# Performance work log

Measured on AMD Instinct MI355X. Metric: run time of the kernel, lower is better.

The kernel has to match this reference:

```python
import jax, jax.numpy as jnp
import numpy as np

R_HEADS = 4   # read heads
CELL = 64     # cell_size (word width)
MEM = 512     # nr_cells
DELTA = 1e-6


def _content_weights(mem, keys, strengths):
    # mem: (B,M,Wc), keys: (B,K,Wc), strengths: (B,K) -> (B,K,M)
    mn = jnp.linalg.norm(mem, axis=2, keepdims=True) + DELTA
    kn = jnp.linalg.norm(keys, axis=2, keepdims=True) + DELTA
    d = jnp.einsum('bkw,bmw->bkm', keys / kn, mem / mn)  # cosine similarity
    return jax.nn.softmax(d * strengths[:, :, None], axis=2)


def _allocate(usage):
    # usage: (B,M) -> allocation weighting (B,M)
    B = usage.shape[0]
    u = DELTA + (1.0 - DELTA) * usage
    idx = jnp.argsort(u, axis=1)                               # ascending usage
    sorted_u = jnp.take_along_axis(u, idx, axis=1)
    prod_su = jnp.cumprod(
        jnp.concatenate([jnp.ones((B, 1), u.dtype), sorted_u], axis=1), axis=1)[:, :-1]
    sorted_alloc = (1.0 - sorted_u) * prod_su
    inv = jnp.argsort(idx, axis=1)                             # inverse permutation
    return jnp.take_along_axis(sorted_alloc, inv, axis=1)


def dnc_forward(x, W_ih, b_ih, W_hh, b_hh, W_out, b_out, W_int, b_int, W_mem, b_mem):
    B, T, IN = x.shape
    H = W_hh.shape[1]
    r, w, m = R_HEADS, CELL, MEM
    eye_mask = 1.0 - jnp.eye(m, dtype=x.dtype)  # zero link-matrix diagonal

    def step(carry, x_t):
        h, c, mem, link, prec, read_w, write_w, usage, last_read = carry
        # controller LSTM cell (torch gate order i,f,g,o)
        inp = jnp.concatenate([x_t, last_read], axis=1)
        gates = inp @ W_ih.T + b_ih + h @ W_hh.T + b_hh
        gi, gf, gg, go = jnp.split(gates, 4, axis=1)
        c = jax.nn.sigmoid(gf) * c + jax.nn.sigmoid(gi) * jnp.tanh(gg)
        h = jax.nn.sigmoid(go) * jnp.tanh(c)
        out = h @ W_out.T + b_out
        xi = h @ W_int.T + b_int  # interface vector, size r*w+3w+5r+3
        # parse interface
        o = r * w
        read_keys = jnp.tanh(xi[:, :r * w].reshape(B, r, w))
        read_str = jax.nn.softplus(xi[:, o:o + r]); o += r
        write_key = jnp.tanh(xi[:, o:o + w].reshape(B, 1, w)); o += w
        write_str = jax.nn.softplus(xi[:, o:o + 1]); o += 1
        erase = jax.nn.sigmoid(xi[:, o:o + w].reshape(B, 1, w)); o += w
        write_vec = jnp.tanh(xi[:, o:o + w].reshape(B, 1, w)); o += w
        free_gates = jax.nn.sigmoid(xi[:, o:o + r]); o += r
        alloc_gate = jax.nn.sigmoid(xi[:, o:o + 1]); o += 1
        write_gate = jax.nn.sigmoid(xi[:, o:o + 1]); o += 1
        read_modes = jax.nn.softmax(xi[:, o:o + 3 * r].reshape(B, r, 3), axis=-1)

        # ---- write ----
        usage = usage + (1 - usage) * (1 - jnp.prod(1 - write_w, axis=1))
        psi = jnp.prod(1 - free_gates[:, :, None] * read_w, axis=1)
        usage = usage * psi
        wcw = _content_weights(mem, write_key, write_str)      # (B,1,M)
        alloc = _allocate(usage)[:, None, :]                   # (B,1,M)
        ag = alloc_gate[:, :, None]
        write_w = write_gate[:, :, None] * (ag * alloc + (1 - ag) * wcw)
        reset = jnp.prod(1 - write_w[:, :, :, None] * erase[:, :, None, :], axis=1)  # (B,M,Wc)
        mem = mem * reset + jnp.einsum('bkm,bkw->bmw', write_w, write_vec)
        ww = write_w[:, 0]                                     # (B,M), single write head
        L = link[:, 0]
        L = (1 - ww[:, :, None] - ww[:, None, :]) * L + ww[:, :, None] * prec[:, 0][:, None, :]
        L = L * eye_mask
        link = L[:, None]
        prec = (1 - jnp.sum(write_w, axis=2, keepdims=True)) * prec + write_w

        # ---- read ----
        cw = _content_weights(mem, read_keys, read_str)        # (B,R,M)
        fwd = jnp.einsum('bij,brj->bri', L, read_w)
        bwd = jnp.einsum('bri,bij->brj', read_w, L)
        read_w = (read_modes[:, :, 0:1] * bwd
                  + read_modes[:, :, 1:2] * fwd
                  + read_modes[:, :, 2:3] * cw)
        read_vecs = jnp.einsum('brm,bmw->brw', read_w, mem).reshape(B, r * w)
        y = jnp.concatenate([out, read_vecs], axis=1) @ W_mem.T + b_mem
        return (h, c, mem, link, prec, read_w, write_w, usage, read_vecs), y

    z = lambda *s: jnp.zeros(s, x.dtype)
    carry0 = (z(B, H), z(B, H), z(B, m, w), z(B, 1, m, m), z(B, 1, m),
              z(B, r, m), z(B, 1, m), z(B, m), z(B, r * w))
    _, ys = jax.lax.scan(step, carry0, jnp.swapaxes(x, 0, 1))
    return jnp.swapaxes(ys, 0, 1)  # (B,T,IN)


def setup_inputs() -> dict:
    key = jax.random.key(0)
    ks = jax.random.split(key, 12)
    B, T, IN, H = 16, 32, 256, 512
    r, w = R_HEADS, CELL
    iface = w * r + 3 * w + 5 * r + 3  # 471
    s = 0.05
    return {
        'x': jax.random.normal(ks[0], (B, T, IN), jnp.float32),
        'W_ih': jax.random.normal(ks[1], (4 * H, IN + r * w), jnp.float32) * s,
        'b_ih': jax.random.normal(ks[2], (4 * H,), jnp.float32) * s,
        'W_hh': jax.random.normal(ks[3], (4 * H, H), jnp.float32) * s,
        'b_hh': jax.random.normal(ks[4], (4 * H,), jnp.float32) * s,
        'W_out': jax.random.normal(ks[5], (H, H), jnp.float32) * s,
        'b_out': jax.random.normal(ks[6], (H,), jnp.float32) * s,
        'W_int': jax.random.normal(ks[7], (iface, H), jnp.float32) * s,
        'b_int': jax.random.normal(ks[8], (iface,), jnp.float32) * s,
        'W_mem': jax.random.normal(ks[9], (IN, r * w + H), jnp.float32) * s,
        'b_mem': jax.random.normal(ks[10], (IN,), jnp.float32) * s,
    }


def reference(x, W_ih, b_ih, W_hh, b_hh, W_out, b_out, W_int, b_int, W_mem, b_mem):
    return dnc_forward(x, W_ih, b_ih, W_hh, b_hh, W_out, b_out, W_int, b_int, W_mem, b_mem)
```

## Files before the change

### kernel.cpp

```cpp
#include <hip/hip_runtime.h>
#include <math.h>

#define NB 16
#define NT 256
#define NWG 256
#define TT 32
#define INP 256
#define HH 512
#define RH 4
#define CWID 64
#define MM 512
#define IFACE 471
#define DELTA 1e-6f
#define AP 516

__device__ __align__(16) float g_h[2][NB][HH];
__device__ __align__(16) float g_c[NB][HH];
__device__ __align__(16) float g_lr[NB][INP];
__device__ __align__(16) float g_usage[NB][MM];
__device__ __align__(16) float g_ww[NB][MM];
__device__ __align__(16) float g_prec[2][NB][MM];
__device__ __align__(16) float g_rw[NB][RH][MM];
__device__ __align__(16) float g_mem[NB][MM][CWID];
__device__ __align__(16) float g_L[NB][MM][MM];
__device__ __align__(16) float g_out[NB][HH];
__device__ __align__(16) float g_xi[NB][HH];
__device__ __align__(16) float g_rkn[NB][RH][CWID];
__device__ __align__(16) float g_rs[NB][RH];
__device__ __align__(16) float g_erase[NB][CWID];
__device__ __align__(16) float g_wv[NB][CWID];
__device__ __align__(16) float g_modes[NB][RH][3];
__device__ __align__(16) float g_fwd[NB][RH][MM];
__device__ __align__(16) float g_bwdp[NB][16][RH][MM];
__device__ __align__(16) float g_e[NB][RH][MM];
__device__ __align__(16) float g_cwsp[NB][16][RH];
__device__ __align__(16) float g_rvp[NB][16][RH][CWID];

struct P {
  const float *x, *W_ih, *b_ih, *W_hh, *b_hh, *W_out, *b_out, *W_int, *b_int, *W_mem, *b_mem;
  float* y;
};

__device__ __forceinline__ float sigf(float x)  { return 1.f / (1.f + __expf(-x)); }
__device__ __forceinline__ float splus(float x) { return fmaxf(x, 0.f) + log1pf(__expf(-fabsf(x))); }

__device__ __forceinline__ void zfill(float* a, long n) {
  const long stride = (long)gridDim.x * blockDim.x;
  for (long i = (long)blockIdx.x * blockDim.x + threadIdx.x; i < n; i += stride) a[i] = 0.f;
}

__global__ void __launch_bounds__(NT) k_init() {
  zfill(&g_h[0][0][0], 2L*NB*HH);
  zfill(&g_c[0][0], (long)NB*HH);
  zfill(&g_lr[0][0], (long)NB*INP);
  zfill(&g_usage[0][0], (long)NB*MM);
  zfill(&g_ww[0][0], (long)NB*MM);
  zfill(&g_prec[0][0][0], 2L*NB*MM);
  zfill(&g_rw[0][0][0], (long)NB*RH*MM);
  zfill(&g_mem[0][0][0], (long)NB*MM*CWID);
  zfill(&g_L[0][0][0], (long)NB*MM*MM);
}

__global__ void __launch_bounds__(NT) k_ph1(P p, int t) {
  __shared__ __align__(16) float sm[14432];
  float* As  = sm;
  float* Ws  = sm + 16*AP;
  float* red = sm + 24*AP;
  const int tid = threadIdx.x;
  const int j0  = 2 * (int)blockIdx.x;
  const int op  = tid & 3;
  const int bq  = (tid >> 2) & 3;
  const int ks  = tid >> 4;
  const float (*hsrc)[HH] = g_h[t & 1];
  float acc0[4] = {0.f,0.f,0.f,0.f};
  float acc1[4] = {0.f,0.f,0.f,0.f};
  for (int pass = 0; pass < 2; ++pass) {
    if (pass == 0) {
      for (int idx = tid; idx < NB*INP; idx += NT) {
        int b = idx >> 8, k = idx & 255;
        As[b*AP + k] = p.x[((size_t)b*TT + t)*INP + k];
      }
      for (int idx = tid; idx < NB*INP; idx += NT) {
        int b = idx >> 8, k = idx & 255;
        As[b*AP + INP + k] = g_lr[b][k];
      }
    } else {
      for (int idx = tid; idx < NB*HH; idx += NT) {
        int b = idx >> 9, k = idx & 511;
        As[b*AP + k] = hsrc[b][k];
      }
    }
    const float* Wsrc = pass ? p.W_hh : p.W_ih;
    for (int idx = tid; idx < 8*512; idx += NT) {
      int ro = idx >> 9, k = idx & 511;
      int row = (ro >> 1)*HH + j0 + (ro & 1);
      Ws[ro*AP + k] = Wsrc[(size_t)row*512 + k];
    }
    __syncthreads();
    const int k0 = ks * 32;
    #pragma unroll
    for (int k4 = 0; k4 < 32; k4 += 4) {
      const float4 w0 = *(const float4*)&Ws[(op*2+0)*AP + k0 + k4];
      const float4 w1 = *(const float4*)&Ws[(op*2+1)*AP + k0 + k4];
      #pragma unroll
      for (int bb = 0; bb < 4; ++bb) {
        const float4 a = *(const float4*)&As[(bq*4+bb)*AP + k0 + k4];
        acc0[bb] += a.x*w0.x + a.y*w0.y + a.z*w0.z + a.w*w0.w;
        acc1[bb] += a.x*w1.x + a.y*w1.y + a.z*w1.z + a.w*w1.w;
      }
    }
    __syncthreads();
  }
  #pragma unroll
  for (int bb = 0; bb < 4; ++bb) {
    red[(op*2+0)*256 + (bq*4+bb)*16 + ks] = acc0[bb];
    red[(op*2+1)*256 + (bq*4+bb)*16 + ks] = acc1[bb];
  }
  __syncthreads();
  if (tid < 128) {
    int o = tid >> 4, b = tid & 15;
    float s = 0.f;
    #pragma unroll
    for (int q = 0; q < 16; ++q) s += red[o*256 + b*16 + q];
    int row = (o >> 1)*HH + j0 + (o & 1);
    red[o*256 + b*16] = s + p.b_ih[row] + p.b_hh[row];
  }
  __syncthreads();
  if (tid < 32) {
    int jj = tid >> 4, b = tid & 15;
    int j  = j0 + jj;
    float gi = red[(0+jj)*256 + b*16];
    float gf = red[(2+jj)*256 + b*16];
    float gg = red[(4+jj)*256 + b*16];
    float go = red[(6+jj)*256 + b*16];
    float c0 = g_c[b][j];
    float cn = sigf(gf)*c0 + sigf(gi)*tanhf(gg);
    float hn = sigf(go)*tanhf(cn);
    g_c[b][j] = cn;
    g_h[(t+1) & 1][b][j] = hn;
  }
}

__global__ void __launch_bounds__(NT) k_ph2(P p, int t) {
  __shared__ __align__(16) float sm[10576];
  float* hs  = sm;
  float* Ws  = sm + 16*AP;
  float* red = sm + 20*AP;
  const int tid = threadIdx.x;
  const int o0  = 4 * (int)blockIdx.x;
  const float (*hcur)[HH] = g_h[(t+1) & 1];
  for (int idx = tid; idx < NB*HH; idx += NT) {
    int b = idx >> 9, k = idx & 511;
    hs[b*AP + k] = hcur[b][k];
  }
  for (int idx = tid; idx < 4*512; idx += NT) {
    int oi = idx >> 9, k = idx & 511;
    int o = o0 + oi;
    float v = 0.f;
    if (o < HH)              v = p.W_out[(size_t)o*512 + k];
    else if (o < HH + IFACE) v = p.W_int[(size_t)(o - HH)*512 + k];
    Ws[oi*AP + k] = v;
  }
  __syncthreads();
  {
    const int b = tid & 15, oi = (tid >> 4) & 3, ks = tid >> 6;
    const int k0 = ks * 128;
    float acc = 0.f;
    #pragma unroll 8
    for (int k4 = 0; k4 < 128; k4 += 4) {
      const float4 a  = *(const float4*)&hs[b*AP + k0 + k4];
      const float4 wv = *(const float4*)&Ws[oi*AP + k0 + k4];
      acc += a.x*wv.x + a.y*wv.y + a.z*wv.z + a.w*wv.w;
    }
    red[(oi*16 + b)*4 + ks] = acc;
  }
  __syncthreads();
  if (tid < 64) {
    int oi = tid >> 4, b = tid & 15;
    int base = (oi*16 + b)*4;
    float s = red[base] + red[base+1] + red[base+2] + red[base+3];
    int o = o0 + oi;
    if (o < HH) g_out[b][o] = s + p.b_out[o];
    else if (o < HH + IFACE) g_xi[b][o - HH] = s + p.b_int[o - HH];
  }
}

__global__ void __launch_bounds__(512) k_ph3(int pp) {
  __shared__ __align__(16) float sm[4152];
  const int b = (int)blockIdx.x, tid = threadIdx.x;
  float* xi_l = sm;
  float* wkn  = sm + 472;
  float* sc   = sm + 536;
  float* u_l  = sm + 552;
  float* wcw  = sm + 1064;
  float* su   = sm + 1576;
  float* cA   = sm + 2088;
  float* cB   = sm + 2600;
  float* wwl  = sm + 3112;
  float* red  = sm + 3624;
  int*   rnk  = (int*)(sm + 3640);

  for (int i = tid; i < IFACE; i += 512) xi_l[i] = g_xi[b][i];
  __syncthreads();
  {
    const int wv = tid >> 6, v = tid & 63;
    if (wv < 4) {
      float kv = tanhf(xi_l[wv*64 + v]);
      float ss = kv * kv;
      #pragma unroll
      for (int d = 1; d < 64; d <<= 1) ss += __shfl_xor(ss, d, 64);
      g_rkn[b][wv][v] = kv / (sqrtf(ss) + DELTA);
      if (v == 0) { float s_ = splus(xi_l[256 + wv]); sc[wv] = s_; g_rs[b][wv] = s_; }
    } else if (wv == 4) {
      float kv = tanhf(xi_l[260 + v]);
      float ss = kv * kv;
      #pragma unroll
      for (int d = 1; d < 64; d <<= 1) ss += __shfl_xor(ss, d, 64);
      wkn[v] = kv / (sqrtf(ss) + DELTA);
    } else if (wv == 5) {
      g_erase[b][v] = sigf(xi_l[325 + v]);
    } else if (wv == 6) {
      g_wv[b][v] = tanhf(xi_l[389 + v]);
    } else {
      if (v < 4)       sc[4 + v] = sigf(xi_l[453 + v]);
      else if (v == 4) sc[8] = sigf(xi_l[457]);
      else if (v == 5) sc[9] = sigf(xi_l[458]);
      else if (v == 6) sc[10] = splus(xi_l[324]);
      else if (v >= 8 && v < 12) {
        int r = v - 8;
        float a0 = xi_l[459 + r*3], a1 = xi_l[459 + r*3 + 1], a2 = xi_l[459 + r*3 + 2];
        float mx = fmaxf(a0, fmaxf(a1, a2));
        float e0 = __expf(a0 - mx), e1 = __expf(a1 - mx), e2 = __expf(a2 - mx);
        float si = e0 + e1 + e2;
        g_modes[b][r][0] = e0/si; g_modes[b][r][1] = e1/si; g_modes[b][r][2] = e2/si;
      }
    }
  }
  __syncthreads();
  {
    float uo = g_usage[b][tid];
    float wwp = g_ww[b][tid];
    float psi = 1.f;
    #pragma unroll
    for (int r = 0; r < RH; ++r) psi *= 1.f - sc[4+r]*g_rw[b][r][tid];
    float un = (uo + (1.f - uo)*wwp) * psi;
    g_usage[b][tid] = un;
    u_l[tid] = DELTA + (1.f - DELTA)*un;
  }
  {
    float dot = 0.f, nn = 0.f;
    const float* mr = &g_mem[b][tid][0];
    #pragma unroll
    for (int v4 = 0; v4 < CWID; v4 += 4) {
      float4 m4 = *(const float4*)&mr[v4];
      dot += m4.x*wkn[v4] + m4.y*wkn[v4+1] + m4.z*wkn[v4+2] + m4.w*wkn[v4+3];
      nn  += m4.x*m4.x + m4.y*m4.y + m4.z*m4.z + m4.w*m4.w;
    }
    wcw[tid] = (dot / (sqrtf(nn) + DELTA)) * sc[10];
  }
  __syncthreads();
  {
    const int wv = tid >> 6, v = tid & 63;
    float x0 = wcw[tid];
    float mx = x0;
    #pragma unroll
    for (int d = 1; d < 64; d <<= 1) mx = fmaxf(mx, __shfl_xor(mx, d, 64));
    if (v == 0) red[wv] = mx;
    __syncthreads();
    float gmx = red[0];
    #pragma unroll
    for (int q = 1; q < 8; ++q) gmx = fmaxf(gmx, red[q]);
    float e0 = __expf(x0 - gmx);
    float ss = e0;
    #pragma unroll
    for (int d = 1; d < 64; d <<= 1) ss += __shfl_xor(ss, d, 64);
    if (v == 0) red[8 + wv] = ss;
    __syncthreads();
    float tot = red[8];
    #pragma unroll
    for (int q = 9; q < 16; ++q) tot += red[q];
    wcw[tid] = e0 / tot;
  }
  __syncthreads();
  {
    const float u0 = u_l[tid];
    int cnt = 0;
    for (int j = 0; j < MM; j += 8) {
      const float4 a = *(const float4*)&u_l[j];
      const float4 c = *(const float4*)&u_l[j + 4];
      cnt += (a.x < u0) || (a.x == u0 && (j+0) < tid);
      cnt += (a.y < u0) || (a.y == u0 && (j+1) < tid);
      cnt += (a.z < u0) || (a.z == u0 && (j+2) < tid);
      cnt += (a.w < u0) || (a.w == u0 && (j+3) < tid);
      cnt += (c.x < u0) || (c.x == u0 && (j+4) < tid);
      cnt += (c.y < u0) || (c.y == u0 && (j+5) < tid);
      cnt += (c.z < u0) || (c.z == u0 && (j+6) < tid);
      cnt += (c.w < u0) || (c.w == u0 && (j+7) < tid);
    }
    rnk[tid] = cnt;
    su[cnt] = u0;
  }
  __syncthreads();
  cA[tid] = tid ? su[tid - 1] : 1.f;
  __syncthreads();
  {
    float* src = cA;
    float* dst = cB;
    for (int d = 1; d < MM; d <<= 1) {
      float v = src[tid];
      if (tid >= d) v *= src[tid - d];
      dst[tid] = v;
      __syncthreads();
      float* tmp = src; src = dst; dst = tmp;
    }
    float ag = sc[8], wgt = sc[9];
    float alloc = (1.f - u_l[tid]) * src[rnk[tid]];
    float wn = wgt * (ag*alloc + (1.f - ag)*wcw[tid]);
    wwl[tid] = wn;
    g_ww[b][tid] = wn;
  }
  __syncthreads();
  {
    const int wv = tid >> 6, v = tid & 63;
    float s2 = wwl[tid];
    #pragma unroll
    for (int d = 1; d < 64; d <<= 1) s2 += __shfl_xor(s2, d, 64);
    if (v == 0) red[wv] = s2;
    __syncthreads();
    float sww = red[0];
    #pragma unroll
    for (int q = 1; q < 8; ++q) sww += red[q];
    g_prec[1 - pp][b][tid] = (1.f - sww)*g_prec[pp][b][tid] + wwl[tid];
  }
}

__global__ void __launch_bounds__(NT) k_ph4(int pp) {
  __shared__ __align__(16) float sm[6608];
  const int w = (int)blockIdx.x, tid = threadIdx.x;
  const int b = w >> 4, s = w & 15, i0 = s * 32;
  float* pl   = sm;
  float* wwl  = sm + 512;
  float* rwl  = sm + 1024;
  float* el   = sm + 3072;
  float* wvl  = sm + 3136;
  float* rknl = sm + 3200;
  float* rs4  = sm + 3456;
  float* fp   = sm + 3472;
  float* mt   = sm + 4496;
  float* nrm  = sm + 6576;

  for (int i = tid; i < MM; i += NT) { pl[i] = g_prec[pp][b][i]; wwl[i] = g_ww[b][i]; }
  for (int i = tid; i < RH*MM; i += NT) rwl[i] = g_rw[b][i >> 9][i & 511];
  for (int i = tid; i < CWID; i += NT) { el[i] = g_erase[b][i]; wvl[i] = g_wv[b][i]; }
  for (int i = tid; i < RH*CWID; i += NT) rknl[i] = g_rkn[b][i >> 6][i & 63];
  if (tid < 4) rs4[tid] = g_rs[b][tid];
  __syncthreads();
  {
    const int ii = tid >> 3, js = tid & 7;
    const int i = i0 + ii;
    const float wwi = wwl[i];
    float f0=0.f, f1=0.f, f2=0.f, f3=0.f;
    float* Lrow = &g_L[b][i][0];
    #pragma unroll
    for (int step = 0; step < 16; ++step) {
      const int col = js*64 + ((js*8 + step*4) & 63);
      float4 l4 = *(float4*)&Lrow[col];
      float lv[4] = {l4.x, l4.y, l4.z, l4.w};
      #pragma unroll
      for (int q = 0; q < 4; ++q) {
        const int jq = col + q;
        float lnv = (1.f - wwi - wwl[jq]) * lv[q] + wwi * pl[jq];
        if (jq == i) lnv = 0.f;
        lv[q] = lnv;
        f0 += lnv * rwl[jq];
        f1 += lnv * rwl[512 + jq];
        f2 += lnv * rwl[1024 + jq];
        f3 += lnv * rwl[1536 + jq];
      }
      *(float4*)&Lrow[col] = make_float4(lv[0], lv[1], lv[2], lv[3]);
    }
    fp[(ii*8 + js)*4 + 0] = f0;
    fp[(ii*8 + js)*4 + 1] = f1;
    fp[(ii*8 + js)*4 + 2] = f2;
    fp[(ii*8 + js)*4 + 3] = f3;
  }
  __syncthreads();
  if (tid < 128) {
    int ii = tid >> 2, r = tid & 3;
    float sY = 0.f;
    #pragma unroll
    for (int js = 0; js < 8; ++js) sY += fp[(ii*8 + js)*4 + r];
    g_fwd[b][r][i0 + ii] = sY;
  }
  {
    const int j = tid * 2;
    float a00=0,a01=0,a10=0,a11=0,a20=0,a21=0,a30=0,a31=0;
    #pragma unroll 4
    for (int ii2 = 0; ii2 < 32; ++ii2) {
      const int i = i0 + ii2;
      const float2 l2 = *(const float2*)&g_L[b][i][j];
      const float r0 = rwl[i], r1 = rwl[512+i], r2 = rwl[1024+i], r3 = rwl[1536+i];
      a00 += r0*l2.x; a01 += r0*l2.y;
      a10 += r1*l2.x; a11 += r1*l2.y;
      a20 += r2*l2.x; a21 += r2*l2.y;
      a30 += r3*l2.x; a31 += r3*l2.y;
    }
    g_bwdp[b][s][0][j] = a00; g_bwdp[b][s][0][j+1] = a01;
    g_bwdp[b][s][1][j] = a10; g_bwdp[b][s][1][j+1] = a11;
    g_bwdp[b][s][2][j] = a20; g_bwdp[b][s][2][j+1] = a21;
    g_bwdp[b][s][3][j] = a30; g_bwdp[b][s][3][j+1] = a31;
  }
  for (int idx = tid; idx < 32*CWID; idx += NT) {
    int ii = idx >> 6, v = idx & 63;
    int i = i0 + ii;
    float wwi = wwl[i];
    float mv = g_mem[b][i][v];
    float mn = mv * (1.f - wwi*el[v]) + wwi*wvl[v];
    g_mem[b][i][v] = mn;
    mt[ii*65 + v] = mn;
  }
  __syncthreads();
  {
    int ii = tid >> 3, js = tid & 7;
    float nn = 0.f;
    #pragma unroll
    for (int q = 0; q < 8; ++q) { float mv = mt[ii*65 + js*8 + q]; nn += mv*mv; }
    fp[(ii*8 + js)*4] = nn;
  }
  __syncthreads();
  if (tid < 32) {
    float nn = 0.f;
    #pragma unroll
    for (int q = 0; q < 8; ++q) nn += fp[(tid*8 + q)*4];
    nrm[tid] = sqrtf(nn) + DELTA;
  }
  __syncthreads();
  {
    int ii = tid >> 3, js = tid & 7;
    float p0=0,p1=0,p2=0,p3=0;
    #pragma unroll
    for (int q = 0; q < 8; ++q) {
      float mv = mt[ii*65 + js*8 + q];
      p0 += mv * rknl[ 0 + js*8 + q];
      p1 += mv * rknl[ 64 + js*8 + q];
      p2 += mv * rknl[128 + js*8 + q];
      p3 += mv * rknl[192 + js*8 + q];
    }
    fp[(ii*8 + js)*4 + 0] = p0;
    fp[(ii*8 + js)*4 + 1] = p1;
    fp[(ii*8 + js)*4 + 2] = p2;
    fp[(ii*8 + js)*4 + 3] = p3;
  }
  __syncthreads();
  if (tid < 128) {
    int ii = tid >> 2, r = tid & 3;
    float d = 0.f;
    #pragma unroll
    for (int js = 0; js < 8; ++js) d += fp[(ii*8 + js)*4 + r];
    float e = __expf((d / nrm[ii]) * rs4[r]);
    g_e[b][r][i0 + ii] = e;
    mt[ii*4 + r] = e;
  }
  __syncthreads();
  if (tid < 4) {
    float ssum = 0.f;
    #pragma unroll
    for (int q = 0; q < 32; ++q) ssum += mt[q*4 + tid];
    g_cwsp[b][s][tid] = ssum;
  }
}

__global__ void __launch_bounds__(NT) k_ph5() {
  __shared__ __align__(16) float sm[144];
  const int w = (int)blockIdx.x, tid = threadIdx.x;
  const int b = w >> 4, s = w & 15, j0 = s * 32;
  float* Sr  = sm;
  float* rwt = sm + 16;
  if (tid < 4) {
    float ss = 0.f;
    #pragma unroll
    for (int q = 0; q < 16; ++q) ss += g_cwsp[b][q][tid];
    Sr[tid] = ss;
  }
  __syncthreads();
  if (tid < 128) {
    int jj = tid >> 2, r = tid & 3;
    int j = j0 + jj;
    float bw = 0.f;
    #pragma unroll
    for (int q = 0; q < 16; ++q) bw += g_bwdp[b][q][r][j];
    float fw = g_fwd[b][r][j];
    float cwv = g_e[b][r][j] / Sr[r];
    float rn = g_modes[b][r][0]*bw + g_modes[b][r][1]*fw + g_modes[b][r][2]*cwv;
    g_rw[b][r][j] = rn;
    rwt[r*32 + jj] = rn;
  }
  __syncthreads();
  {
    int r = tid >> 6, v = tid & 63;
    float acc = 0.f;
    #pragma unroll
    for (int jj = 0; jj < 32; ++jj) acc += rwt[r*32 + jj] * g_mem[b][j0 + jj][v];
    g_rvp[b][s][r][v] = acc;
  }
}

__global__ void __launch_bounds__(NT) k_ph6(P p, int t) {
  __shared__ __align__(16) float sm[1024];
  const int w = (int)blockIdx.x, tid = threadIdx.x;
  const int b = w >> 4, s = w & 15, o0 = s * 16;
  float* rv   = sm;
  float* outl = sm + 256;
  float* red  = sm + 768;
  {
    int r = tid >> 6, v = tid & 63;
    float acc = 0.f;
    #pragma unroll
    for (int q = 0; q < 16; ++q) acc += g_rvp[b][q][r][v];
    rv[r*64 + v] = acc;
    if (s == 0) g_lr[b][r*64 + v] = acc;
  }
  for (int k = tid; k < HH; k += NT) outl[k] = g_out[b][k];
  __syncthreads();
  {
    int oi = tid & 15, ks = tid >> 4;
    int o = o0 + oi;
    const float* wm = &p.W_mem[(size_t)o * 768];
    float acc = 0.f;
    for (int k = ks*48; k < ks*48 + 48; ++k) {
      float a = (k < HH) ? outl[k] : rv[k - HH];
      acc += a * wm[k];
    }
    red[oi*16 + ks] = acc;
  }
  __syncthreads();
  if (tid < 16) {
    int o = o0 + tid;
    float ss = 0.f;
    #pragma unroll
    for (int q = 0; q < 16; ++q) ss += red[tid*16 + q];
    p.y[((size_t)b*TT + t)*INP + o] = ss + p.b_mem[o];
  }
}

extern "C" void kernel_launch(void* const* d_in, const int* in_sizes, int n_in,
                              void* d_out, int out_size, void* d_ws, size_t ws_size,
                              hipStream_t stream) {
  (void)in_sizes; (void)n_in; (void)out_size; (void)d_ws; (void)ws_size;
  P p;
  p.x     = (const float*)d_in[0];
  p.W_ih  = (const float*)d_in[1];
  p.b_ih  = (const float*)d_in[2];
  p.W_hh  = (const float*)d_in[3];
  p.b_hh  = (const float*)d_in[4];
  p.W_out = (const float*)d_in[5];
  p.b_out = (const float*)d_in[6];
  p.W_int = (const float*)d_in[7];
  p.b_int = (const float*)d_in[8];
  p.W_mem = (const float*)d_in[9];
  p.b_mem = (const float*)d_in[10];
  p.y     = (float*)d_out;

  k_init<<<dim3(1024), dim3(NT), 0, stream>>>();
  for (int t = 0; t < TT; ++t) {
    const int pp = t & 1;
    k_ph1<<<dim3(NWG), dim3(NT), 0, stream>>>(p, t);
    k_ph2<<<dim3(NWG), dim3(NT), 0, stream>>>(p, t);
    k_ph3<<<dim3(NB),  dim3(512), 0, stream>>>(pp);
    k_ph4<<<dim3(NWG), dim3(NT), 0, stream>>>(pp);
    k_ph5<<<dim3(NWG), dim3(NT), 0, stream>>>();
    k_ph6<<<dim3(NWG), dim3(NT), 0, stream>>>(p, t);
  }
}
```

Baseline: 2.182 ms.

## Fuse read-weight and output phases, warp-scan cumprod, nontemporal weight loads

```diff
diff --git a/kernel.cpp b/kernel.cpp
--- a/kernel.cpp
+++ b/kernel.cpp
@@ -13,6 +13,8 @@
 #define IFACE 471
 #define DELTA 1e-6f
 #define AP 516
+
+#define NTLOAD(p_) __builtin_nontemporal_load(p_)
 
 __device__ __align__(16) float g_h[2][NB][HH];
 __device__ __align__(16) float g_c[NB][HH];
@@ -34,7 +36,6 @@
 __device__ __align__(16) float g_bwdp[NB][16][RH][MM];
 __device__ __align__(16) float g_e[NB][RH][MM];
 __device__ __align__(16) float g_cwsp[NB][16][RH];
-__device__ __align__(16) float g_rvp[NB][16][RH][CWID];
 
 struct P {
   const float *x, *W_ih, *b_ih, *W_hh, *b_hh, *W_out, *b_out, *W_int, *b_int, *W_mem, *b_mem;
@@ -94,7 +95,7 @@
     for (int idx = tid; idx < 8*512; idx += NT) {
       int ro = idx >> 9, k = idx & 511;
       int row = (ro >> 1)*HH + j0 + (ro & 1);
-      Ws[ro*AP + k] = Wsrc[(size_t)row*512 + k];
+      Ws[ro*AP + k] = NTLOAD(&Wsrc[(size_t)row*512 + k]);
     }
     __syncthreads();
     const int k0 = ks * 32;
@@ -157,8 +158,8 @@
     int oi = idx >> 9, k = idx & 511;
     int o = o0 + oi;
     float v = 0.f;
-    if (o < HH)              v = p.W_out[(size_t)o*512 + k];
-    else if (o < HH + IFACE) v = p.W_int[(size_t)(o - HH)*512 + k];
+    if (o < HH)              v = NTLOAD(&p.W_out[(size_t)o*512 + k]);
+    else if (o < HH + IFACE) v = NTLOAD(&p.W_int[(size_t)(o - HH)*512 + k]);
     Ws[oi*AP + k] = v;
   }
   __syncthreads();
@@ -194,7 +195,6 @@
   float* u_l  = sm + 552;
   float* wcw  = sm + 1064;
   float* su   = sm + 1576;
-  float* cA   = sm + 2088;
   float* cB   = sm + 2600;
   float* wwl  = sm + 3112;
   float* red  = sm + 3624;
@@ -301,20 +301,24 @@
     su[cnt] = u0;
   }
   __syncthreads();
-  cA[tid] = tid ? su[tid - 1] : 1.f;
-  __syncthreads();
-  {
-    float* src = cA;
-    float* dst = cB;
-    for (int d = 1; d < MM; d <<= 1) {
-      float v = src[tid];
-      if (tid >= d) v *= src[tid - d];
-      dst[tid] = v;
-      __syncthreads();
-      float* tmp = src; src = dst; dst = tmp;
-    }
+  {
+    const int lane = tid & 63, wv = tid >> 6;
+    float v = su[tid];
+    #pragma unroll
+    for (int d = 1; d < 64; d <<= 1) {
+      float m = __shfl_up(v, d, 64);
+      if (lane >= d) v *= m;
+    }
+    if (lane == 63) red[wv] = v;
+    __syncthreads();
+    float pre = 1.f;
+    for (int q = 0; q < wv; ++q) pre *= red[q];
+    cB[tid] = v * pre;
+    __syncthreads();
     float ag = sc[8], wgt = sc[9];
-    float alloc = (1.f - u_l[tid]) * src[rnk[tid]];
+    int rk = rnk[tid];
+    float excl = rk ? cB[rk - 1] : 1.f;
+    float alloc = (1.f - u_l[tid]) * excl;
     float wn = wgt * (ag*alloc + (1.f - ag)*wcw[tid]);
     wwl[tid] = wn;
     g_ww[b][tid] = wn;
@@ -470,57 +474,44 @@
   }
 }
 
-__global__ void __launch_bounds__(NT) k_ph5() {
-  __shared__ __align__(16) float sm[144];
+__global__ void __launch_bounds__(NT) k_ph56(P p, int t) {
+  __shared__ __align__(16) float sm[3072];
   const int w = (int)blockIdx.x, tid = threadIdx.x;
-  const int b = w >> 4, s = w & 15, j0 = s * 32;
-  float* Sr  = sm;
-  float* rwt = sm + 16;
-  if (tid < 4) {
+  const int b = w >> 4, s = w & 15, o0 = s * 16;
+  float* rwl  = sm;
+  float* rvl  = sm + 2048;
+  float* outl = sm + 2304;
+  float* red  = sm + 2816;
+  float Sr[4];
+  #pragma unroll
+  for (int r = 0; r < 4; ++r) {
     float ss = 0.f;
     #pragma unroll
-    for (int q = 0; q < 16; ++q) ss += g_cwsp[b][q][tid];
-    Sr[tid] = ss;
-  }
-  __syncthreads();
-  if (tid < 128) {
-    int jj = tid >> 2, r = tid & 3;
-    int j = j0 + jj;
-    float bw = 0.f;
-    #pragma unroll
-    for (int q = 0; q < 16; ++q) bw += g_bwdp[b][q][r][j];
-    float fw = g_fwd[b][r][j];
-    float cwv = g_e[b][r][j] / Sr[r];
-    float rn = g_modes[b][r][0]*bw + g_modes[b][r][1]*fw + g_modes[b][r][2]*cwv;
-    g_rw[b][r][j] = rn;
-    rwt[r*32 + jj] = rn;
-  }
+    for (int q = 0; q < 16; ++q) ss += g_cwsp[b][q][r];
+    Sr[r] = ss;
+  }
+  for (int jj = tid; jj < MM; jj += NT) {
+    #pragma unroll
+    for (int r = 0; r < 4; ++r) {
+      float bw = 0.f;
+      #pragma unroll
+      for (int q = 0; q < 16; ++q) bw += g_bwdp[b][q][r][jj];
+      float fw = g_fwd[b][r][jj];
+      float cwv = g_e[b][r][jj] / Sr[r];
+      float rn = g_modes[b][r][0]*bw + g_modes[b][r][1]*fw + g_modes[b][r][2]*cwv;
+      rwl[r*512 + jj] = rn;
+      if (s == 0) g_rw[b][r][jj] = rn;
+    }
+  }
+  for (int k = tid; k < HH; k += NT) outl[k] = g_out[b][k];
   __syncthreads();
   {
     int r = tid >> 6, v = tid & 63;
     float acc = 0.f;
-    #pragma unroll
-    for (int jj = 0; jj < 32; ++jj) acc += rwt[r*32 + jj] * g_mem[b][j0 + jj][v];
-    g_rvp[b][s][r][v] = acc;
-  }
-}
-
-__global__ void __launch_bounds__(NT) k_ph6(P p, int t) {
-  __shared__ __align__(16) float sm[1024];
-  const int w = (int)blockIdx.x, tid = threadIdx.x;
-  const int b = w >> 4, s = w & 15, o0 = s * 16;
-  float* rv   = sm;
-  float* outl = sm + 256;
-  float* red  = sm + 768;
-  {
-    int r = tid >> 6, v = tid & 63;
-    float acc = 0.f;
-    #pragma unroll
-    for (int q = 0; q < 16; ++q) acc += g_rvp[b][q][r][v];
-    rv[r*64 + v] = acc;
+    for (int j = 0; j < MM; ++j) acc += rwl[r*512 + j] * g_mem[b][j][v];
+    rvl[r*64 + v] = acc;
     if (s == 0) g_lr[b][r*64 + v] = acc;
   }
-  for (int k = tid; k < HH; k += NT) outl[k] = g_out[b][k];
   __syncthreads();
   {
     int oi = tid & 15, ks = tid >> 4;
@@ -528,8 +519,8 @@
     const float* wm = &p.W_mem[(size_t)o * 768];
     float acc = 0.f;
     for (int k = ks*48; k < ks*48 + 48; ++k) {
-      float a = (k < HH) ? outl[k] : rv[k - HH];
-      acc += a * wm[k];
+      float a = (k < HH) ? outl[k] : rvl[k - HH];
+      acc += a * NTLOAD(&wm[k]);
     }
     red[oi*16 + ks] = acc;
   }
@@ -568,7 +559,6 @@
     k_ph2<<<dim3(NWG), dim3(NT), 0, stream>>>(p, t);
     k_ph3<<<dim3(NB),  dim3(512), 0, stream>>>(pp);
     k_ph4<<<dim3(NWG), dim3(NT), 0, stream>>>(pp);
-    k_ph5<<<dim3(NWG), dim3(NT), 0, stream>>>();
-    k_ph6<<<dim3(NWG), dim3(NT), 0, stream>>>(p, t);
-  }
-}
+    k_ph56<<<dim3(NWG), dim3(NT), 0, stream>>>(p, t);
+  }
+}
```

Measured after the change: 3.015 ms. +38.2%, slower.
